# Kernel optimization log

Measured on AMD Instinct MI355X. Metric: run time of the kernel, lower is better.

The kernel has to match this reference:

```python
import jax, jax.numpy as jnp
import numpy as np
import math

NHEAD = 8
IOU_THR = 0.2
COS_THR = 0.2


def _build_mask(segments, q):
    # segments: [bz, Lq, 2] (center, length); q: [bz, Lq, d]
    c, l = segments[..., 0], segments[..., 1]
    s, e = c - l / 2, c + l / 2  # ml2se: midpoint-length -> start-end
    inter = jnp.clip(jnp.minimum(e[:, :, None], e[:, None, :])
                     - jnp.maximum(s[:, :, None], s[:, None, :]), 0.0)
    union = l[:, :, None] + l[:, None, :] - inter
    iou = inter / union  # [bz, Lq, Lq]
    qn = q / jnp.maximum(jnp.linalg.norm(q, axis=-1, keepdims=True), 1e-8)
    cos = jnp.einsum('bid,bjd->bij', qn, qn)
    Lq = q.shape[1]
    adj = jnp.broadcast_to(jnp.eye(Lq, dtype=bool), iou.shape)
    adj = jnp.where(iou <= IOU_THR, True, adj)   # adj_matrix[iou<=0.2]=1
    adj = jnp.where(cos <= COS_THR, False, adj)  # adj_matrix[cos<=0.2]=0
    return ~adj  # True = masked


def setup_inputs() -> dict:
    key = jax.random.key(0)
    ks = jax.random.split(key, 8)
    Lq, bz, d = 1024, 8, 512
    bound = 1.0 / math.sqrt(d)
    query = jax.random.normal(ks[0], (Lq, bz, d), jnp.float32)
    segments = jax.random.uniform(ks[1], (bz, Lq, 2), jnp.float32)
    Wq = jax.random.uniform(ks[2], (d, d), jnp.float32, -bound, bound)
    bq = jax.random.uniform(ks[3], (d,), jnp.float32, -bound, bound)
    Wk = jax.random.uniform(ks[4], (d, d), jnp.float32, -bound, bound)
    bk = jax.random.uniform(ks[5], (d,), jnp.float32, -bound, bound)
    Wv = jax.random.uniform(ks[6], (d, d), jnp.float32, -bound, bound)
    bv = jax.random.uniform(ks[7], (d,), jnp.float32, -bound, bound)
    return dict(query=query, segments=segments, Wq=Wq, bq=bq, Wk=Wk, bk=bk,
                Wv=Wv, bv=bv)


def reference(query, segments, Wq, bq, Wk, bk, Wv, bv):
    Lq, bz, d = query.shape
    dh = d // NHEAD
    h = jnp.transpose(query, (1, 0, 2))  # [bz, Lq, d]
    mask = _build_mask(segments, h)      # [bz, Lq, Lq], bool
    Q = (h @ Wq.T + bq).reshape(bz, Lq, NHEAD, dh)
    K = (h @ Wk.T + bk).reshape(bz, Lq, NHEAD, dh)
    V = (h @ Wv.T + bv).reshape(bz, Lq, NHEAD, dh)
    scores = jnp.einsum('bihd,bjhd->bhij', Q, K) / math.sqrt(dh)
    scores = jnp.where(mask[:, None, :, :], -jnp.inf, scores)
    attn = jax.nn.softmax(scores, axis=-1)
    out = jnp.einsum('bhij,bjhd->bihd', attn, V).reshape(bz, Lq, d) + h
    return jnp.transpose(out, (1, 0, 2))  # [Lq, bz, d]
```

## Files before the change

kernel.cpp:

```cpp
#include <hip/hip_runtime.h>
#include <math.h>

#define LQ 1024
#define BZ 8
#define D  512
#define NH 8
#define DH 64
#define IOU_THR 0.2f
#define COS_THR 0.2f
#define NEG (-1e30f)
#define FIXCAP 16384

typedef short bf16x8 __attribute__((ext_vector_type(8)));
typedef float f32x4  __attribute__((ext_vector_type(4)));

#define MFMA16(a, b, cacc) __builtin_amdgcn_mfma_f32_16x16x32_bf16(a, b, cacc, 0, 0, 0)

__device__ inline unsigned short f2bf(float x) {
    union { float f; unsigned int u; } v; v.f = x;
    unsigned int r = v.u + 0x7FFF + ((v.u >> 16) & 1);
    return (unsigned short)(r >> 16);
}

__device__ __forceinline__ void gll16(const void* g, void* ldsbase) {
    __builtin_amdgcn_global_load_lds(
        (const __attribute__((address_space(1))) unsigned int*)g,
        (__attribute__((address_space(3))) unsigned int*)ldsbase, 16, 0, 0);
}

__global__ __launch_bounds__(256) void prep_kernel(const float* __restrict__ query,
                                                   const float* __restrict__ Wq,
                                                   const float* __restrict__ Wk,
                                                   const float* __restrict__ Wv,
                                                   unsigned short* __restrict__ hi,
                                                   unsigned short* __restrict__ Wb,
                                                   float* __restrict__ rnorm) {
    int blk = blockIdx.x, tid = threadIdx.x;
    if (blk < 2048) {
        int w = tid >> 6, lane = tid & 63;
        int row = blk * 4 + w;
        int b = row >> 10, i = row & 1023;
        const float* src = query + ((size_t)i * BZ + b) * D + lane * 8;
        float4 v0 = *(const float4*)src;
        float4 v1 = *(const float4*)(src + 4);
        uint4 pk;
        pk.x = (unsigned)f2bf(v0.x) | ((unsigned)f2bf(v0.y) << 16);
        pk.y = (unsigned)f2bf(v0.z) | ((unsigned)f2bf(v0.w) << 16);
        pk.z = (unsigned)f2bf(v1.x) | ((unsigned)f2bf(v1.y) << 16);
        pk.w = (unsigned)f2bf(v1.z) | ((unsigned)f2bf(v1.w) << 16);
        *(uint4*)(hi + (size_t)row * D + lane * 8) = pk;
        float ss = v0.x * v0.x + v0.y * v0.y + v0.z * v0.z + v0.w * v0.w
                 + v1.x * v1.x + v1.y * v1.y + v1.z * v1.z + v1.w * v1.w;
        #pragma unroll
        for (int s = 1; s < 64; s <<= 1) ss += __shfl_xor(ss, s);
        if (lane == 0) rnorm[row] = 1.0f / fmaxf(sqrtf(ss), 1e-8f);
    } else {
        int t = (blk - 2048) * 256 + tid;
        int mat = t >> 16;
        int off = (t & 65535) * 4;
        const float* src = (mat == 0) ? Wq : (mat == 1) ? Wk : Wv;
        float4 v = *(const float4*)(src + off);
        uint2 p;
        p.x = (unsigned)f2bf(v.x) | ((unsigned)f2bf(v.y) << 16);
        p.y = (unsigned)f2bf(v.z) | ((unsigned)f2bf(v.w) << 16);
        *(uint2*)(Wb + (size_t)mat * D * D + off) = p;
    }
}

__global__ __launch_bounds__(256) void gemm_kernel(const unsigned short* __restrict__ hi,
                                                   const unsigned short* __restrict__ Wb,
                                                   const float* __restrict__ rnorm,
                                                   const float* __restrict__ segments,
                                                   const float* __restrict__ bq,
                                                   const float* __restrict__ bk,
                                                   const float* __restrict__ bv,
                                                   unsigned char* __restrict__ mask,
                                                   unsigned char* __restrict__ summ,
                                                   int* __restrict__ fix_cnt,
                                                   unsigned int* __restrict__ fix_list,
                                                   unsigned short* __restrict__ Qb,
                                                   unsigned short* __restrict__ Kb,
                                                   unsigned short* __restrict__ Vt) {
    __shared__ short As[128 * 64], Bs[128 * 64];
    __shared__ float4 iSE[128], jSE[128];
    __shared__ int summ_lds[8][2];
    int blk = blockIdx.x, tid = threadIdx.x, w = tid >> 6, lane = tid & 63;
    int c = lane & 15, q4 = lane >> 4;
    int wr = w >> 1, wc = w & 1;

    bool is_qkv = blk < 768;
    const char *Asrc, *Bsrc;
    int b = 0, i0 = 0, j0 = 0, z = 0, m0 = 0, n0 = 0;
    if (is_qkv) {
        z = blk >> 8; int rem = blk & 255;
        m0 = (rem >> 2) * 128; n0 = (rem & 3) * 128;
        Asrc = (const char*)(hi + (size_t)m0 * D);
        Bsrc = (const char*)(Wb + (size_t)z * D * D + (size_t)n0 * D);
    } else {
        int id2 = blk - 768;
        b = id2 >> 6; i0 = ((id2 >> 3) & 7) * 128; j0 = (id2 & 7) * 128;
        Asrc = (const char*)(hi + ((size_t)b * LQ + i0) * D);
        Bsrc = (const char*)(hi + ((size_t)b * LQ + j0) * D);
        if (tid < 16) summ_lds[tid >> 1][tid & 1] = 0;
    }

    int rgrp = lane >> 3;
    int qg   = (lane & 7) ^ (rgrp & 7);
    size_t lgoff = (size_t)rgrp * 1024 + (size_t)qg * 16;
    int swz = c & 7;

    f32x4 acc[4][4] = {};
    for (int k0 = 0; k0 < D; k0 += 64) {
        size_t kb = (size_t)k0 * 2;
        #pragma unroll
        for (int m = 0; m < 4; m++) {
            int n = 4 * w + m;
            gll16(Asrc + kb + (size_t)n * 8192 + lgoff, (char*)As + n * 1024);
            gll16(Bsrc + kb + (size_t)n * 8192 + lgoff, (char*)Bs + n * 1024);
        }
        __syncthreads();
        #pragma unroll
        for (int s = 0; s < 2; s++) {
            bf16x8 af[4], bf[4];
            #pragma unroll
            for (int f = 0; f < 4; f++) {
                af[f] = *(const bf16x8*)&As[(wr * 64 + f * 16 + c) * 64 + ((s * 4 + q4) ^ swz) * 8];
                bf[f] = *(const bf16x8*)&Bs[(wc * 64 + f * 16 + c) * 64 + ((s * 4 + q4) ^ swz) * 8];
            }
            #pragma unroll
            for (int fr = 0; fr < 4; fr++)
                #pragma unroll
                for (int fc = 0; fc < 4; fc++)
                    acc[fr][fc] = MFMA16(af[fr], bf[fc], acc[fr][fc]);
        }
        __syncthreads();
    }

    if (is_qkv) {
        const float* bias = (z == 0) ? bq : (z == 1) ? bk : bv;
        #pragma unroll
        for (int fr = 0; fr < 4; fr++)
            #pragma unroll
            for (int r = 0; r < 4; r++) {
                int m = m0 + wr * 64 + fr * 16 + q4 * 4 + r;
                int bb = m >> 10, i = m & 1023;
                #pragma unroll
                for (int fc = 0; fc < 4; fc++) {
                    int n = n0 + wc * 64 + fc * 16 + c;
                    unsigned short us = f2bf(acc[fr][fc][r] + bias[n]);
                    int hh = n >> 6, dh = n & 63;
                    size_t bh = (size_t)bb * NH + hh;
                    if (z == 2)
                        Vt[(bh * DH + dh) * LQ + i] = us;
                    else {
                        unsigned short* dst = (z == 0) ? Qb : Kb;
                        dst[(bh * LQ + i) * DH + dh] = us;
                    }
                }
            }
    } else {
        const float2* seg2 = (const float2*)(segments + (size_t)b * LQ * 2);
        const float* rn = rnorm + b * LQ;
        if (tid < 128) {
            float2 cl = seg2[i0 + tid];
            iSE[tid] = make_float4(cl.x - cl.y * 0.5f, cl.x + cl.y * 0.5f, cl.y, rn[i0 + tid]);
        } else {
            float2 cl = seg2[j0 + tid - 128];
            jSE[tid - 128] = make_float4(cl.x - cl.y * 0.5f, cl.x + cl.y * 0.5f, cl.y, rn[j0 + tid - 128]);
        }
        __syncthreads();

        unsigned char* mbase = mask + ((size_t)b << 20);
        #pragma unroll
        for (int fr = 0; fr < 4; fr++) {
            int anyun = 0;
            #pragma unroll
            for (int r = 0; r < 4; r++) {
                int il = wr * 64 + fr * 16 + q4 * 4 + r;
                int i = i0 + il;
                float4 I = iSE[il];
                #pragma unroll
                for (int fc = 0; fc < 4; fc++) {
                    int jl = wc * 64 + fc * 16 + c;
                    int j = j0 + jl;
                    float4 J = jSE[jl];
                    float cosv = acc[fr][fc][r] * I.w * J.w;
                    if (fabsf(cosv - COS_THR) < 1.5e-3f) {
                        int idx = atomicAdd(fix_cnt, 1);
                        if (idx < FIXCAP)
                            fix_list[idx] = ((unsigned int)b << 20) | ((unsigned int)i << 10) | j;
                    }
                    float inter = fmaxf(fminf(I.y, J.y) - fmaxf(I.x, J.x), 0.0f);
                    float uni   = I.z + J.z - inter;
                    float iou   = inter / uni;
                    bool adj = ((iou <= IOU_THR) || (i == j)) && (cosv > COS_THR);
                    mbase[(size_t)i * LQ + j] = adj ? 0 : 1;
                    anyun |= adj ? 1 : 0;
                }
            }
            if (anyun) atomicOr(&summ_lds[wr * 4 + fr][wc], 1);
        }
        __syncthreads();
        if (tid < 16) {
            int lit = tid >> 1, ljt = tid & 1;
            summ[((size_t)b * 64 + (i0 >> 4) + lit) * 16 + (j0 >> 6) + ljt] =
                summ_lds[lit][ljt] ? 1 : 0;
        }
    }
}

__global__ __launch_bounds__(64) void fixup_kernel(const float* __restrict__ query,
                                                   const float* __restrict__ rnorm,
                                                   const float* __restrict__ segments,
                                                   const int* __restrict__ fix_cnt,
                                                   const unsigned int* __restrict__ fix_list,
                                                   unsigned char* __restrict__ mask,
                                                   unsigned char* __restrict__ summ) {
    int cnt = *fix_cnt; if (cnt > FIXCAP) cnt = FIXCAP;
    int lane = threadIdx.x;
    for (int e = blockIdx.x; e < cnt; e += gridDim.x) {
        unsigned int pk = fix_list[e];
        int b = pk >> 20, i = (pk >> 10) & 1023, j = pk & 1023;
        const float* hri = query + ((size_t)i * BZ + b) * D;
        const float* hrj = query + ((size_t)j * BZ + b) * D;
        double dd = 0.0;
        #pragma unroll
        for (int k = 0; k < D / 64; k++)
            dd += (double)hri[k * 64 + lane] * (double)hrj[k * 64 + lane];
        #pragma unroll
        for (int s = 1; s < 64; s <<= 1) dd += __shfl_xor(dd, s);
        if (lane == 0) {
            float rni = rnorm[b * LQ + i], rnj = rnorm[b * LQ + j];
            float cosv = (float)(dd * (double)rni * (double)rnj);
            const float* seg = segments + (size_t)b * LQ * 2;
            float ci = seg[i * 2], li = seg[i * 2 + 1];
            float cj = seg[j * 2], lj = seg[j * 2 + 1];
            float si = ci - li * 0.5f, ei = ci + li * 0.5f;
            float sj = cj - lj * 0.5f, ej = cj + lj * 0.5f;
            float inter = fmaxf(fminf(ei, ej) - fmaxf(si, sj), 0.0f);
            float iou = inter / (li + lj - inter);
            bool adj = ((iou <= IOU_THR) || (i == j)) && (cosv > COS_THR);
            mask[((size_t)b * LQ + i) * LQ + j] = adj ? 0 : 1;
            if (adj) summ[((size_t)b * 64 + (i >> 4)) * 16 + (j >> 6)] = 1;
        }
    }
}

__global__ __launch_bounds__(256) void attn_kernel(const unsigned short* __restrict__ Qb,
                                                   const unsigned short* __restrict__ Kb,
                                                   const unsigned short* __restrict__ Vt,
                                                   const unsigned char* __restrict__ mask,
                                                   const unsigned char* __restrict__ summ,
                                                   const float* __restrict__ query,
                                                   float* __restrict__ out) {
    int tid = threadIdx.x;
    int w = tid >> 6, lane = tid & 63;
    int c = lane & 15, q4 = lane >> 4;
    int hh = blockIdx.y, b = blockIdx.z;
    int i0 = blockIdx.x * 64 + w * 16;
    size_t bh = (size_t)b * NH + hh;

    __shared__ unsigned short p_lds[4][16][72];

    const unsigned short* Qrow = Qb + (bh * LQ + i0 + c) * DH;
    bf16x8 qa0 = *(const bf16x8*)(Qrow + q4 * 8);
    bf16x8 qa1 = *(const bf16x8*)(Qrow + 32 + q4 * 8);

    f32x4 O[4] = {};
    float m_r[4] = {NEG, NEG, NEG, NEG};
    float l_r[4] = {0.f, 0.f, 0.f, 0.f};

    const unsigned short* Kbase = Kb + bh * LQ * DH;
    const unsigned short* Vbase = Vt + bh * DH * LQ;
    const unsigned char*  mbase = mask + ((size_t)b * LQ + i0) * LQ;
    const unsigned char*  srow  = summ + ((size_t)b * 64 + (i0 >> 4)) * 16;

    for (int jt = 0; jt < 16; jt++) {
        if (!srow[jt]) continue;
        int j0 = jt * 64;
        f32x4 S[4] = {};
        #pragma unroll
        for (int cb = 0; cb < 4; cb++) {
            const unsigned short* krow = Kbase + (size_t)(j0 + cb * 16 + c) * DH;
            bf16x8 kf0 = *(const bf16x8*)(krow + q4 * 8);
            bf16x8 kf1 = *(const bf16x8*)(krow + 32 + q4 * 8);
            S[cb] = MFMA16(qa0, kf0, S[cb]);
            S[cb] = MFMA16(qa1, kf1, S[cb]);
        }
        float p[4][4];
        float tmax[4] = {NEG, NEG, NEG, NEG};
        #pragma unroll
        for (int cb = 0; cb < 4; cb++)
            #pragma unroll
            for (int r = 0; r < 4; r++) {
                float sc = S[cb][r] * 0.125f;
                unsigned char mm = mbase[(size_t)(q4 * 4 + r) * LQ + j0 + cb * 16 + c];
                sc = mm ? NEG : sc;
                p[cb][r] = sc;
                tmax[r] = fmaxf(tmax[r], sc);
            }
        #pragma unroll
        for (int r = 0; r < 4; r++) {
            float v = tmax[r];
            v = fmaxf(v, __shfl_xor(v, 1));
            v = fmaxf(v, __shfl_xor(v, 2));
            v = fmaxf(v, __shfl_xor(v, 4));
            v = fmaxf(v, __shfl_xor(v, 8));
            tmax[r] = v;
        }
        float rsum[4];
        #pragma unroll
        for (int r = 0; r < 4; r++) {
            float mn = fmaxf(m_r[r], tmax[r]);
            float alpha = __expf(m_r[r] - mn);
            m_r[r] = mn;
            l_r[r] *= alpha;
            #pragma unroll
            for (int cb2 = 0; cb2 < 4; cb2++) O[cb2][r] *= alpha;
            float s0 = 0.f;
            #pragma unroll
            for (int cb = 0; cb < 4; cb++) {
                float e = __expf(p[cb][r] - mn);
                p[cb][r] = e;
                s0 += e;
            }
            rsum[r] = s0;
        }
        #pragma unroll
        for (int r = 0; r < 4; r++) {
            float v = rsum[r];
            v += __shfl_xor(v, 1);
            v += __shfl_xor(v, 2);
            v += __shfl_xor(v, 4);
            v += __shfl_xor(v, 8);
            l_r[r] += v;
        }
        #pragma unroll
        for (int cb = 0; cb < 4; cb++)
            #pragma unroll
            for (int r = 0; r < 4; r++)
                p_lds[w][q4 * 4 + r][cb * 16 + c] = f2bf(p[cb][r]);
        #pragma unroll
        for (int s = 0; s < 2; s++) {
            bf16x8 pf = *(const bf16x8*)&p_lds[w][c][s * 32 + q4 * 8];
            #pragma unroll
            for (int cb = 0; cb < 4; cb++) {
                bf16x8 vf = *(const bf16x8*)(Vbase + (size_t)(cb * 16 + c) * LQ + j0 + s * 32 + q4 * 8);
                O[cb] = MFMA16(pf, vf, O[cb]);
            }
        }
    }
    #pragma unroll
    for (int r = 0; r < 4; r++) {
        int i = i0 + q4 * 4 + r;
        float inv = 1.0f / l_r[r];
        #pragma unroll
        for (int cb = 0; cb < 4; cb++) {
            int col = hh * 64 + cb * 16 + c;
            size_t oidx = ((size_t)i * BZ + b) * D + col;
            out[oidx] = O[cb][r] * inv + query[oidx];
        }
    }
}

extern "C" void kernel_launch(void* const* d_in, const int* in_sizes, int n_in,
                              void* d_out, int out_size, void* d_ws, size_t ws_size,
                              hipStream_t stream) {
    const float* query    = (const float*)d_in[0];
    const float* segments = (const float*)d_in[1];
    const float* Wq = (const float*)d_in[2];
    const float* bq = (const float*)d_in[3];
    const float* Wk = (const float*)d_in[4];
    const float* bk = (const float*)d_in[5];
    const float* Wv = (const float*)d_in[6];
    const float* bv = (const float*)d_in[7];
    float* out = (float*)d_out;

    const size_t NTOK = (size_t)BZ * LQ;
    char* ws = (char*)d_ws;
    unsigned short* hbuf  = (unsigned short*)ws;   ws += NTOK * D * 2;
    unsigned short* Qb    = (unsigned short*)ws;   ws += NTOK * D * 2;
    unsigned short* Kb    = (unsigned short*)ws;   ws += NTOK * D * 2;
    unsigned short* Vt    = (unsigned short*)ws;   ws += NTOK * D * 2;
    unsigned short* Wb    = (unsigned short*)ws;   ws += (size_t)3 * D * D * 2;
    float*          rnorm = (float*)ws;            ws += NTOK * 4;
    unsigned char*  mask  = (unsigned char*)ws;    ws += (size_t)BZ * LQ * LQ;
    unsigned char*  summ  = (unsigned char*)ws;    ws += 8192;
    int*            fix_cnt = (int*)ws;            ws += 64;
    unsigned int*   fix_list = (unsigned int*)ws;

    hipMemsetAsync(fix_cnt, 0, 64, stream);
    prep_kernel<<<2816, 256, 0, stream>>>(query, Wq, Wk, Wv, hbuf, Wb, rnorm);
    gemm_kernel<<<1280, 256, 0, stream>>>(hbuf, Wb, rnorm, segments, bq, bk, bv,
                                          mask, summ, fix_cnt, fix_list, Qb, Kb, Vt);
    fixup_kernel<<<64, 64, 0, stream>>>(query, rnorm, segments, fix_cnt, fix_list, mask, summ);
    attn_kernel<<<dim3(LQ / 64, NH, BZ), 256, 0, stream>>>(Qb, Kb, Vt, mask, summ, query, out);
}
```

Before: 160.5 us.

## Exploit symmetry of cosine/IoU mask to compute only upper-triangular tiles

The mask is symmetric in i and j, so the mask-GEMM part now launches only the upper-triangular 128x128 tile pairs (36 per batch instead of 64). Each off-diagonal tile writes both its own mask entries and the transposed ones, packing four bytes per store, and updates the transposed summary bits as well. The fixup kernel also writes both symmetric entries. This cuts the Gram-matrix GEMM work by close to half, at the cost of strided transposed byte stores and some index arithmetic.

Measured after the change: 160.2 us. No clear change (-0.2%).

```diff
diff --git a/kernel.cpp b/kernel.cpp
--- a/kernel.cpp
+++ b/kernel.cpp
@@ -83,7 +83,7 @@
                                                    unsigned short* __restrict__ Vt) {
     __shared__ short As[128 * 64], Bs[128 * 64];
     __shared__ float4 iSE[128], jSE[128];
-    __shared__ int summ_lds[8][2];
+    __shared__ int summ_lds[8][2], summ_t_lds[8][2];
     int blk = blockIdx.x, tid = threadIdx.x, w = tid >> 6, lane = tid & 63;
     int c = lane & 15, q4 = lane >> 4;
     int wr = w >> 1, wc = w & 1;
@@ -98,10 +98,18 @@
         Bsrc = (const char*)(Wb + (size_t)z * D * D + (size_t)n0 * D);
     } else {
         int id2 = blk - 768;
-        b = id2 >> 6; i0 = ((id2 >> 3) & 7) * 128; j0 = (id2 & 7) * 128;
+        b = id2 / 36;
+        int t = id2 - b * 36;
+        int it = 0;
+        while (t >= 8 - it) { t -= 8 - it; it++; }
+        int jt = it + t;
+        i0 = it * 128; j0 = jt * 128;
         Asrc = (const char*)(hi + ((size_t)b * LQ + i0) * D);
         Bsrc = (const char*)(hi + ((size_t)b * LQ + j0) * D);
-        if (tid < 16) summ_lds[tid >> 1][tid & 1] = 0;
+        if (tid < 16) {
+            summ_lds[tid >> 1][tid & 1] = 0;
+            summ_t_lds[tid >> 1][tid & 1] = 0;
+        }
     }
 
     int rgrp = lane >> 3;
@@ -170,10 +178,13 @@
         }
         __syncthreads();
 
+        bool offdiag = (i0 != j0);
         unsigned char* mbase = mask + ((size_t)b << 20);
+        int anyT[4] = {0, 0, 0, 0};
         #pragma unroll
         for (int fr = 0; fr < 4; fr++) {
             int anyun = 0;
+            unsigned int tpack[4] = {0, 0, 0, 0};
             #pragma unroll
             for (int r = 0; r < 4; r++) {
                 int il = wr * 64 + fr * 16 + q4 * 4 + r;
@@ -195,16 +206,34 @@
                     float iou   = inter / uni;
                     bool adj = ((iou <= IOU_THR) || (i == j)) && (cosv > COS_THR);
                     mbase[(size_t)i * LQ + j] = adj ? 0 : 1;
+                    tpack[fc] |= (adj ? 0u : 1u) << (8 * r);
                     anyun |= adj ? 1 : 0;
+                    anyT[fc] |= adj ? 1 : 0;
                 }
             }
             if (anyun) atomicOr(&summ_lds[wr * 4 + fr][wc], 1);
+            if (offdiag) {
+                int ibase = i0 + wr * 64 + fr * 16 + q4 * 4;
+                #pragma unroll
+                for (int fc = 0; fc < 4; fc++) {
+                    int j = j0 + wc * 64 + fc * 16 + c;
+                    *(unsigned int*)&mbase[(size_t)j * LQ + ibase] = tpack[fc];
+                }
+            }
+        }
+        if (offdiag) {
+            #pragma unroll
+            for (int fc = 0; fc < 4; fc++)
+                if (anyT[fc]) atomicOr(&summ_t_lds[wc * 4 + fc][wr], 1);
         }
         __syncthreads();
         if (tid < 16) {
             int lit = tid >> 1, ljt = tid & 1;
             summ[((size_t)b * 64 + (i0 >> 4) + lit) * 16 + (j0 >> 6) + ljt] =
                 summ_lds[lit][ljt] ? 1 : 0;
+            if (offdiag)
+                summ[((size_t)b * 64 + (j0 >> 4) + lit) * 16 + (i0 >> 6) + ljt] =
+                    summ_t_lds[lit][ljt] ? 1 : 0;
         }
     }
 }
@@ -240,8 +269,13 @@
             float inter = fmaxf(fminf(ei, ej) - fmaxf(si, sj), 0.0f);
             float iou = inter / (li + lj - inter);
             bool adj = ((iou <= IOU_THR) || (i == j)) && (cosv > COS_THR);
-            mask[((size_t)b * LQ + i) * LQ + j] = adj ? 0 : 1;
-            if (adj) summ[((size_t)b * 64 + (i >> 4)) * 16 + (j >> 6)] = 1;
+            unsigned char mv = adj ? 0 : 1;
+            mask[((size_t)b * LQ + i) * LQ + j] = mv;
+            mask[((size_t)b * LQ + j) * LQ + i] = mv;
+            if (adj) {
+                summ[((size_t)b * 64 + (i >> 4)) * 16 + (j >> 6)] = 1;
+                summ[((size_t)b * 64 + (j >> 4)) * 16 + (i >> 6)] = 1;
+            }
         }
     }
 }
@@ -391,7 +425,7 @@
 
     hipMemsetAsync(fix_cnt, 0, 64, stream);
     prep_kernel<<<2816, 256, 0, stream>>>(query, Wq, Wk, Wv, hbuf, Wb, rnorm);
-    gemm_kernel<<<1280, 256, 0, stream>>>(hbuf, Wb, rnorm, segments, bq, bk, bv,
+    gemm_kernel<<<1056, 256, 0, stream>>>(hbuf, Wb, rnorm, segments, bq, bk, bv,
                                           mask, summ, fix_cnt, fix_list, Qb, Kb, Vt);
     fixup_kernel<<<64, 64, 0, stream>>>(query, rnorm, segments, fix_cnt, fix_list, mask, summ);
     attn_kernel<<<dim3(LQ / 64, NH, BZ), 256, 0, stream>>>(Qb, Kb, Vt, mask, summ, query, out);
```
